# Kernel tuning notes

Measured on AMD Instinct MI355X. Metric: run time of the kernel, lower is better.

## Reference

```python
import jax, jax.numpy as jnp
import numpy as np

N = 100000
NNZ = 3200000
NFEAT, NHID, NCLASS = 512, 256, 41

def setup_inputs() -> dict:
    key = jax.random.key(0)
    ks = jax.random.split(key, 8)
    x = jax.random.normal(ks[0], (N, NFEAT), dtype=jnp.float32)
    adj_rows = jnp.sort(jax.random.randint(ks[1], (NNZ,), 0, N))
    adj_cols = jax.random.randint(ks[2], (NNZ,), 0, N)
    adj_vals = jax.random.uniform(ks[3], (NNZ,), dtype=jnp.float32) / 32.0  # ~normalized adj
    s1 = 1.0 / np.sqrt(NHID)
    s2 = 1.0 / np.sqrt(NCLASS)
    w1 = jax.random.uniform(ks[4], (NFEAT, NHID), minval=-s1, maxval=s1, dtype=jnp.float32)
    b1 = jax.random.uniform(ks[5], (NHID,), minval=-s1, maxval=s1, dtype=jnp.float32)
    w2 = jax.random.uniform(ks[6], (NHID, NCLASS), minval=-s2, maxval=s2, dtype=jnp.float32)
    b2 = jax.random.uniform(ks[7], (NCLASS,), minval=-s2, maxval=s2, dtype=jnp.float32)
    return {"x": x, "adj_rows": adj_rows, "adj_cols": adj_cols, "adj_vals": adj_vals,
            "w1": w1, "b1": b1, "w2": w2, "b2": b2}

def spmm(rows, cols, vals, dense):
    # sparse [N,N] @ dense [N,D] via gather + segment_sum
    gathered = dense[cols] * vals[:, None]  # [nnz, D]
    return jax.ops.segment_sum(gathered, rows, num_segments=N)

def reference(x, adj_rows, adj_cols, adj_vals, w1, b1, w2, b2):
    # layer 1: A(XW) + b, relu  (GraphConvolution)
    h = spmm(adj_rows, adj_cols, adj_vals, x @ w1) + b1
    h = jax.nn.relu(h)
    # dropout: inference mode (training=False) -> identity
    # layer 2: (AX)W + b  (GraphConvolution2)
    out = spmm(adj_rows, adj_cols, adj_vals, h) @ w2 + b2
    return jax.nn.log_softmax(out, axis=1)
```

## Files before the change

kernel.cpp:

```cpp
#include <hip/hip_runtime.h>
#include <math.h>

#define N_NODES 100000
#define NNZ_E   3200000
#define NFEAT   512
#define NHID    256
#define NCLASS  41
#define NC_PAD  48
#define P_STRIDE 64

typedef __attribute__((ext_vector_type(8))) short   short8;
typedef __attribute__((ext_vector_type(8))) unsigned short ushort8;
typedef __attribute__((ext_vector_type(4))) float   f32x4;
typedef __attribute__((ext_vector_type(2))) float   f32x2;

typedef __attribute__((address_space(1))) const unsigned int gu32;
typedef __attribute__((address_space(3))) unsigned int lu32;

__device__ __forceinline__ unsigned short f2bf(float f) {
    unsigned u = __builtin_bit_cast(unsigned, f);
    unsigned r = u + 0x7fffu + ((u >> 16) & 1u);
    return (unsigned short)(r >> 16);
}
__device__ __forceinline__ unsigned char f2fp8(float f) {
    return (unsigned char)(__builtin_amdgcn_cvt_pk_fp8_f32(f, 0.f, 0, false) & 0xff);
}

__global__ __launch_bounds__(256) void prep_x_kernel(const float* __restrict__ x,
                                                     unsigned char* __restrict__ xq) {
    long i = (long)(blockIdx.x * 256 + threadIdx.x) * 16;
    float4 f0 = *(const float4*)(x + i);
    float4 f1 = *(const float4*)(x + i + 4);
    float4 f2 = *(const float4*)(x + i + 8);
    float4 f3 = *(const float4*)(x + i + 12);
    uint4 o;
    o.x = (unsigned)__builtin_amdgcn_cvt_pk_fp8_f32(f0.x, f0.y, 0, false);
    o.x = (unsigned)__builtin_amdgcn_cvt_pk_fp8_f32(f0.z, f0.w, (int)o.x, true);
    o.y = (unsigned)__builtin_amdgcn_cvt_pk_fp8_f32(f1.x, f1.y, 0, false);
    o.y = (unsigned)__builtin_amdgcn_cvt_pk_fp8_f32(f1.z, f1.w, (int)o.y, true);
    o.z = (unsigned)__builtin_amdgcn_cvt_pk_fp8_f32(f2.x, f2.y, 0, false);
    o.z = (unsigned)__builtin_amdgcn_cvt_pk_fp8_f32(f2.z, f2.w, (int)o.z, true);
    o.w = (unsigned)__builtin_amdgcn_cvt_pk_fp8_f32(f3.x, f3.y, 0, false);
    o.w = (unsigned)__builtin_amdgcn_cvt_pk_fp8_f32(f3.z, f3.w, (int)o.w, true);
    *(uint4*)(xq + i) = o;
}

__global__ void prep_w_kernel(const float* __restrict__ w1, const float* __restrict__ w2,
                              unsigned char* __restrict__ w1q, unsigned short* __restrict__ w2t) {
    int tid = blockIdx.x * 256 + threadIdx.x;
    if (tid < NHID * NFEAT) {
        int n = tid >> 9, k = tid & 511;
        w1q[tid] = f2fp8(w1[k * NHID + n]);
    }
    int t2 = tid - NHID * NFEAT;
    if (t2 >= 0 && t2 < NC_PAD * NHID) {
        int n = t2 >> 8, k = t2 & 255;
        w2t[t2] = (n < NCLASS) ? f2bf(w2[k * NCLASS + n]) : (unsigned short)0;
    }
}

__global__ void rowptr_kernel(const int* __restrict__ rows, int* __restrict__ row_ptr) {
    int r = blockIdx.x * 256 + threadIdx.x;
    if (r > N_NODES) return;
    int lo = 0, hi = NNZ_E;
    while (lo < hi) {
        int mid = (lo + hi) >> 1;
        if (rows[mid] < r) lo = mid + 1; else hi = mid;
    }
    row_ptr[r] = lo;
}

__global__ __launch_bounds__(256) void gemm1_kernel(const unsigned char* __restrict__ xq,
                                                    const unsigned char* __restrict__ w1q,
                                                    unsigned char* __restrict__ xw) {
    __shared__ unsigned char As[8192];
    __shared__ unsigned char Bs[8192];

    const int wv   = threadIdx.x >> 6;
    const int lane = threadIdx.x & 63;
    const int l15  = lane & 15;
    const int quad = lane >> 4;
    const int rb   = blockIdx.x * 128;
    const int nb   = blockIdx.y * 128;

    const int srow0 = (wv * 2 + 0) * 16 + (lane >> 2);
    const int srow1 = (wv * 2 + 1) * 16 + (lane >> 2);
    const int g0 = (lane & 3) ^ ((srow0 >> 1) & 3);
    const int g1 = (lane & 3) ^ ((srow1 >> 1) & 3);
    int ga0 = rb + srow0; if (ga0 >= N_NODES) ga0 = N_NODES - 1;
    int ga1 = rb + srow1; if (ga1 >= N_NODES) ga1 = N_NODES - 1;
    const unsigned char* agp0 = xq + (long)ga0 * NFEAT + g0 * 16;
    const unsigned char* agp1 = xq + (long)ga1 * NFEAT + g1 * 16;
    const unsigned char* bgp0 = w1q + (long)(nb + srow0) * NFEAT + g0 * 16;
    const unsigned char* bgp1 = w1q + (long)(nb + srow1) * NFEAT + g1 * 16;

    f32x4 acc[4][4] = {};

    for (int kc = 0; kc < NFEAT; kc += 64) {
        __builtin_amdgcn_global_load_lds((gu32*)(agp0 + kc), (lu32*)(As + (wv * 2 + 0) * 1024), 16, 0, 0);
        __builtin_amdgcn_global_load_lds((gu32*)(agp1 + kc), (lu32*)(As + (wv * 2 + 1) * 1024), 16, 0, 0);
        __builtin_amdgcn_global_load_lds((gu32*)(bgp0 + kc), (lu32*)(Bs + (wv * 2 + 0) * 1024), 16, 0, 0);
        __builtin_amdgcn_global_load_lds((gu32*)(bgp1 + kc), (lu32*)(Bs + (wv * 2 + 1) * 1024), 16, 0, 0);
        __syncthreads();

        unsigned long long a[4][2], b[4][2];
#pragma unroll
        for (int mt = 0; mt < 4; mt++) {
            int row = (wv & 1) * 64 + mt * 16 + l15;
#pragma unroll
            for (int ks = 0; ks < 2; ks++) {
                int p8 = (ks * 4 + quad) ^ (row & 6);
                a[mt][ks] = *(const unsigned long long*)(As + row * 64 + p8 * 8);
            }
        }
#pragma unroll
        for (int nt = 0; nt < 4; nt++) {
            int nr = (wv >> 1) * 64 + nt * 16 + l15;
#pragma unroll
            for (int ks = 0; ks < 2; ks++) {
                int p8 = (ks * 4 + quad) ^ (nr & 6);
                b[nt][ks] = *(const unsigned long long*)(Bs + nr * 64 + p8 * 8);
            }
        }
#pragma unroll
        for (int ks = 0; ks < 2; ks++)
#pragma unroll
            for (int nt = 0; nt < 4; nt++)
#pragma unroll
                for (int mt = 0; mt < 4; mt++)
                    acc[mt][nt] = __builtin_amdgcn_mfma_f32_16x16x32_fp8_fp8(
                        (long)a[mt][ks], (long)b[nt][ks], acc[mt][nt], 0, 0, 0);
        __syncthreads();
    }

#pragma unroll
    for (int mt = 0; mt < 4; mt++) {
        int row0 = rb + (wv & 1) * 64 + mt * 16 + quad * 4;
#pragma unroll
        for (int nt = 0; nt < 4; nt++) {
            int col = nb + (wv >> 1) * 64 + nt * 16 + l15;
#pragma unroll
            for (int r = 0; r < 4; r++) {
                int row = row0 + r;
                if (row < N_NODES)
                    xw[(long)row * NHID + col] = f2fp8(acc[mt][nt][r]);
            }
        }
    }
}

__global__ __launch_bounds__(256) void spmm1_kernel(const unsigned char* __restrict__ xw,
                                                    const int* __restrict__ row_ptr,
                                                    const int* __restrict__ cols,
                                                    const float* __restrict__ vals,
                                                    const float* __restrict__ b1,
                                                    unsigned short* __restrict__ h) {
    int row = blockIdx.x * 4 + (threadIdx.x >> 6);
    if (row >= N_NODES) return;
    int lane = threadIdx.x & 63;
    int e0 = row_ptr[row], e1 = row_ptr[row + 1];

    float a0 = 0.f, a1 = 0.f, a2 = 0.f, a3 = 0.f;
    for (int base = e0; base < e1; base += 64) {
        int   myc = 0;
        float myv = 0.f;
        int idx = base + lane;
        if (idx < e1) { myc = cols[idx]; myv = vals[idx]; }
        int cnt = e1 - base; if (cnt > 64) cnt = 64;
        int j = 0;
        for (; j + 8 <= cnt; j += 8) {
            int c[8]; float v[8];
#pragma unroll
            for (int u = 0; u < 8; u++) { c[u] = __shfl(myc, j + u); v[u] = __shfl(myv, j + u); }
            unsigned q[8];
#pragma unroll
            for (int u = 0; u < 8; u++) q[u] = *(const unsigned*)(xw + (long)c[u] * NHID + lane * 4);
#pragma unroll
            for (int u = 0; u < 8; u++) {
                f32x2 lo = __builtin_amdgcn_cvt_pk_f32_fp8((int)q[u], false);
                f32x2 hi = __builtin_amdgcn_cvt_pk_f32_fp8((int)q[u], true);
                a0 += v[u] * lo[0];
                a1 += v[u] * lo[1];
                a2 += v[u] * hi[0];
                a3 += v[u] * hi[1];
            }
        }
        for (; j < cnt; j++) {
            int   c = __shfl(myc, j);
            float v = __shfl(myv, j);
            unsigned q = *(const unsigned*)(xw + (long)c * NHID + lane * 4);
            f32x2 lo = __builtin_amdgcn_cvt_pk_f32_fp8((int)q, false);
            f32x2 hi = __builtin_amdgcn_cvt_pk_f32_fp8((int)q, true);
            a0 += v * lo[0];
            a1 += v * lo[1];
            a2 += v * hi[0];
            a3 += v * hi[1];
        }
    }
    float4 bv = *(const float4*)(b1 + lane * 4);
    a0 = fmaxf(a0 + bv.x, 0.f);
    a1 = fmaxf(a1 + bv.y, 0.f);
    a2 = fmaxf(a2 + bv.z, 0.f);
    a3 = fmaxf(a3 + bv.w, 0.f);
    uint2 o;
    o.x = (unsigned)f2bf(a0) | ((unsigned)f2bf(a1) << 16);
    o.y = (unsigned)f2bf(a2) | ((unsigned)f2bf(a3) << 16);
    *(uint2*)(h + (long)row * NHID + lane * 4) = o;
}

__global__ __launch_bounds__(256) void gemm2_kernel(const unsigned short* __restrict__ h,
                                                    const unsigned short* __restrict__ w2t,
                                                    unsigned char* __restrict__ p) {
    int rt = blockIdx.x * 4 + (threadIdx.x >> 6);
    int row0 = rt * 16;
    if (row0 >= N_NODES) return;
    int lane = threadIdx.x & 63;
    int l15 = lane & 15, quad = lane >> 4;

    int arow = row0 + l15; if (arow >= N_NODES) arow = N_NODES - 1;
    f32x4 acc[3] = {};
#pragma unroll
    for (int kc = 0; kc < NHID; kc += 32) {
        short8 a = *(const short8*)(h + (long)arow * NHID + kc + quad * 8);
#pragma unroll
        for (int nt = 0; nt < 3; nt++) {
            short8 b = *(const short8*)(w2t + (long)(nt * 16 + l15) * NHID + kc + quad * 8);
            acc[nt] = __builtin_amdgcn_mfma_f32_16x16x32_bf16(a, b, acc[nt], 0, 0, 0);
        }
    }
#pragma unroll
    for (int nt = 0; nt < 3; nt++) {
        int col = nt * 16 + l15;
#pragma unroll
        for (int r = 0; r < 4; r++) {
            int row = row0 + quad * 4 + r;
            if (row < N_NODES)
                p[(long)row * P_STRIDE + col] = f2fp8(acc[nt][r]);
        }
    }
}

__global__ __launch_bounds__(256) void spmm2_kernel(const unsigned char* __restrict__ p,
                                                    const int* __restrict__ row_ptr,
                                                    const int* __restrict__ cols,
                                                    const float* __restrict__ vals,
                                                    const float* __restrict__ b2,
                                                    float* __restrict__ out) {
    int row = blockIdx.x * 4 + (threadIdx.x >> 6);
    if (row >= N_NODES) return;
    int lane = threadIdx.x & 63;
    int e = lane >> 5;
    int t = lane & 31;
    int e0 = row_ptr[row], e1 = row_ptr[row + 1];

    float a0 = 0.f, a1 = 0.f, a2 = 0.f, a3 = 0.f;
    for (int base = e0; base < e1; base += 64) {
        int   myc = 0;
        float myv = 0.f;
        int idx = base + lane;
        if (idx < e1) { myc = cols[idx]; myv = vals[idx]; }
        int cnt = e1 - base; if (cnt > 64) cnt = 64;
        int j = 0;
        for (; j + 8 <= cnt; j += 8) {
            int c[4]; float v[4];
#pragma unroll
            for (int u = 0; u < 4; u++) {
                c[u] = __shfl(myc, j + 2 * u + e);
                v[u] = __shfl(myv, j + 2 * u + e);
            }
            unsigned q[4];
#pragma unroll
            for (int u = 0; u < 4; u++)
                q[u] = (t < 12) ? *(const unsigned*)(p + (long)c[u] * P_STRIDE + 4 * t) : 0u;
#pragma unroll
            for (int u = 0; u < 4; u++) {
                f32x2 lo = __builtin_amdgcn_cvt_pk_f32_fp8((int)q[u], false);
                f32x2 hi = __builtin_amdgcn_cvt_pk_f32_fp8((int)q[u], true);
                a0 += v[u] * lo[0];
                a1 += v[u] * lo[1];
                a2 += v[u] * hi[0];
                a3 += v[u] * hi[1];
            }
        }
        for (; j < cnt; j += 2) {
            int jj = j + e;
            int jc = jj < cnt ? jj : cnt - 1;
            int   c = __shfl(myc, jc);
            float v = __shfl(myv, jc);
            if (jj >= cnt) v = 0.f;
            unsigned q = (t < 12) ? *(const unsigned*)(p + (long)c * P_STRIDE + 4 * t) : 0u;
            f32x2 lo = __builtin_amdgcn_cvt_pk_f32_fp8((int)q, false);
            f32x2 hi = __builtin_amdgcn_cvt_pk_f32_fp8((int)q, true);
            a0 += v * lo[0];
            a1 += v * lo[1];
            a2 += v * hi[0];
            a3 += v * hi[1];
        }
    }
    a0 += __shfl_xor(a0, 32);
    a1 += __shfl_xor(a1, 32);
    a2 += __shfl_xor(a2, 32);
    a3 += __shfl_xor(a3, 32);

    int c0 = 4 * t, c1 = 4 * t + 1, c2 = 4 * t + 2, c3 = 4 * t + 3;
    float l0 = (c0 < NCLASS) ? a0 + b2[c0] : -__builtin_inff();
    float l1 = (c1 < NCLASS) ? a1 + b2[c1] : -__builtin_inff();
    float l2 = (c2 < NCLASS) ? a2 + b2[c2] : -__builtin_inff();
    float l3 = (c3 < NCLASS) ? a3 + b2[c3] : -__builtin_inff();
    float m = fmaxf(fmaxf(l0, l1), fmaxf(l2, l3));
#pragma unroll
    for (int s = 16; s; s >>= 1) m = fmaxf(m, __shfl_xor(m, s));
    float esum = ((c0 < NCLASS) ? __expf(l0 - m) : 0.f)
               + ((c1 < NCLASS) ? __expf(l1 - m) : 0.f)
               + ((c2 < NCLASS) ? __expf(l2 - m) : 0.f)
               + ((c3 < NCLASS) ? __expf(l3 - m) : 0.f);
#pragma unroll
    for (int s = 16; s; s >>= 1) esum += __shfl_xor(esum, s);
    float lse = m + __logf(esum);
    if (e == 0) {
        long ob = (long)row * NCLASS;
        if (c0 < NCLASS) out[ob + c0] = l0 - lse;
        if (c1 < NCLASS) out[ob + c1] = l1 - lse;
        if (c2 < NCLASS) out[ob + c2] = l2 - lse;
        if (c3 < NCLASS) out[ob + c3] = l3 - lse;
    }
}

extern "C" void kernel_launch(void* const* d_in, const int* in_sizes, int n_in,
                              void* d_out, int out_size, void* d_ws, size_t ws_size,
                              hipStream_t stream) {
    const float* x        = (const float*)d_in[0];
    const int*   adj_rows = (const int*)  d_in[1];
    const int*   adj_cols = (const int*)  d_in[2];
    const float* adj_vals = (const float*)d_in[3];
    const float* w1       = (const float*)d_in[4];
    const float* b1       = (const float*)d_in[5];
    const float* w2       = (const float*)d_in[6];
    const float* b2       = (const float*)d_in[7];
    float* out = (float*)d_out;

    char* ws = (char*)d_ws;
    unsigned char*  w1q     = (unsigned char*) (ws);
    unsigned short* w2t     = (unsigned short*)(ws + 0x20000);
    int*            row_ptr = (int*)           (ws + 0x26000);
    unsigned char*  xq      = (unsigned char*) (ws + 0x90000);
    unsigned short* hbuf    = (unsigned short*)(ws + 0x90000);
    unsigned char*  xw      = (unsigned char*) (ws + 0x3180000);
    unsigned char*  p       = (unsigned char*) (ws + 0x3180000);

    prep_x_kernel<<<(N_NODES * NFEAT) / 16 / 256, 256, 0, stream>>>(x, xq);
    prep_w_kernel<<<(NHID * NFEAT + NC_PAD * NHID + 255) / 256, 256, 0, stream>>>(w1, w2, w1q, w2t);
    rowptr_kernel<<<(N_NODES + 1 + 255) / 256, 256, 0, stream>>>(adj_rows, row_ptr);
    gemm1_kernel<<<dim3((N_NODES + 127) / 128, 2), 256, 0, stream>>>(xq, w1q, xw);
    spmm1_kernel<<<(N_NODES + 3) / 4, 256, 0, stream>>>(xw, row_ptr, adj_cols, adj_vals, b1, hbuf);
    gemm2_kernel<<<((N_NODES + 15) / 16 + 3) / 4, 256, 0, stream>>>(hbuf, w2t, p);
    spmm2_kernel<<<(N_NODES + 3) / 4, 256, 0, stream>>>(p, row_ptr, adj_cols, adj_vals, b2, out);
}
```

Baseline: 568.7 us.

## Slice XW into 32-byte column panels and split SpMM1 across slices

GEMM1 now writes its FP8 output as eight column slices of 32 bytes per row. SpMM1 launches eight times as many blocks, one per (row group, slice). In each wave, 8 edge groups of 8 lanes gather 32-byte segments from the slice, with the next column and value loads prefetched, and the partial sums are reduced by cross-lane shuffles. The intent is to shrink each slice's gather working set so it fits better in L2/MALL and to spread edges across lanes, at the cost of reading cols/vals eight times. The row-pointer and weight-prep kernels are merged into one launch, and nontemporal loads are added for the edge arrays.

```diff
diff --git a/kernel.cpp b/kernel.cpp
--- a/kernel.cpp
+++ b/kernel.cpp
@@ -9,10 +9,15 @@
 #define NC_PAD  48
 #define P_STRIDE 64
 
+#define SLICE_B      32
+#define NSLICE       8
+#define SLICE_STRIDE (N_NODES * SLICE_B)
+
 typedef __attribute__((ext_vector_type(8))) short   short8;
 typedef __attribute__((ext_vector_type(8))) unsigned short ushort8;
 typedef __attribute__((ext_vector_type(4))) float   f32x4;
 typedef __attribute__((ext_vector_type(2))) float   f32x2;
+typedef __attribute__((ext_vector_type(2))) unsigned int u32x2;
 
 typedef __attribute__((address_space(1))) const unsigned int gu32;
 typedef __attribute__((address_space(3))) unsigned int lu32;
@@ -45,29 +50,37 @@
     *(uint4*)(xq + i) = o;
 }
 
-__global__ void prep_w_kernel(const float* __restrict__ w1, const float* __restrict__ w2,
-                              unsigned char* __restrict__ w1q, unsigned short* __restrict__ w2t) {
-    int tid = blockIdx.x * 256 + threadIdx.x;
-    if (tid < NHID * NFEAT) {
+__global__ __launch_bounds__(256) void prep_misc_kernel(const int* __restrict__ rows,
+                                                        const float* __restrict__ w1,
+                                                        const float* __restrict__ w2,
+                                                        int* __restrict__ row_ptr,
+                                                        unsigned char* __restrict__ w1q,
+                                                        unsigned short* __restrict__ w2t) {
+    int b = blockIdx.x;
+    if (b < 392) {
+        int r = b * 256 + threadIdx.x;
+        if (r > N_NODES) return;
+        int lo = 0, hi = NNZ_E;
+        while (lo < hi) {
+            int mid = (lo + hi) >> 1;
+            if (rows[mid] < r) lo = mid + 1; else hi = mid;
+        }
+        row_ptr[r] = lo;
+        return;
+    }
+    b -= 392;
+    if (b < 512) {
+        int tid = b * 256 + threadIdx.x;
         int n = tid >> 9, k = tid & 511;
         w1q[tid] = f2fp8(w1[k * NHID + n]);
-    }
-    int t2 = tid - NHID * NFEAT;
-    if (t2 >= 0 && t2 < NC_PAD * NHID) {
+        return;
+    }
+    b -= 512;
+    {
+        int t2 = b * 256 + threadIdx.x;
         int n = t2 >> 8, k = t2 & 255;
         w2t[t2] = (n < NCLASS) ? f2bf(w2[k * NCLASS + n]) : (unsigned short)0;
     }
-}
-
-__global__ void rowptr_kernel(const int* __restrict__ rows, int* __restrict__ row_ptr) {
-    int r = blockIdx.x * 256 + threadIdx.x;
-    if (r > N_NODES) return;
-    int lo = 0, hi = NNZ_E;
-    while (lo < hi) {
-        int mid = (lo + hi) >> 1;
-        if (rows[mid] < r) lo = mid + 1; else hi = mid;
-    }
-    row_ptr[r] = lo;
 }
 
 __global__ __launch_bounds__(256) void gemm1_kernel(const unsigned char* __restrict__ xq,
@@ -139,73 +152,82 @@
 #pragma unroll
         for (int nt = 0; nt < 4; nt++) {
             int col = nb + (wv >> 1) * 64 + nt * 16 + l15;
+            long sb = (long)(col >> 5) * SLICE_STRIDE + (col & 31);
 #pragma unroll
             for (int r = 0; r < 4; r++) {
                 int row = row0 + r;
                 if (row < N_NODES)
-                    xw[(long)row * NHID + col] = f2fp8(acc[mt][nt][r]);
-            }
-        }
-    }
-}
-
-__global__ __launch_bounds__(256) void spmm1_kernel(const unsigned char* __restrict__ xw,
+                    xw[sb + (long)row * SLICE_B] = f2fp8(acc[mt][nt][r]);
+            }
+        }
+    }
+}
+
+__global__ __launch_bounds__(256) void spmm1_kernel(const unsigned char* __restrict__ xws,
                                                     const int* __restrict__ row_ptr,
                                                     const int* __restrict__ cols,
                                                     const float* __restrict__ vals,
                                                     const float* __restrict__ b1,
                                                     unsigned short* __restrict__ h) {
-    int row = blockIdx.x * 4 + (threadIdx.x >> 6);
+    const int slice = blockIdx.x & 7;
+    const int row   = (blockIdx.x >> 3) * 4 + (threadIdx.x >> 6);
     if (row >= N_NODES) return;
-    int lane = threadIdx.x & 63;
-    int e0 = row_ptr[row], e1 = row_ptr[row + 1];
+    const int lane = threadIdx.x & 63;
+    const int e = lane >> 3;
+    const int t = lane & 7;
+    int e0 = __builtin_amdgcn_readfirstlane(row_ptr[row]);
+    int e1 = __builtin_amdgcn_readfirstlane(row_ptr[row + 1]);
+
+    const unsigned char* sbase = xws + (long)slice * SLICE_STRIDE;
+    const unsigned toff = (unsigned)(t << 2);
 
     float a0 = 0.f, a1 = 0.f, a2 = 0.f, a3 = 0.f;
-    for (int base = e0; base < e1; base += 64) {
-        int   myc = 0;
-        float myv = 0.f;
-        int idx = base + lane;
-        if (idx < e1) { myc = cols[idx]; myv = vals[idx]; }
-        int cnt = e1 - base; if (cnt > 64) cnt = 64;
-        int j = 0;
-        for (; j + 8 <= cnt; j += 8) {
-            int c[8]; float v[8];
-#pragma unroll
-            for (int u = 0; u < 8; u++) { c[u] = __shfl(myc, j + u); v[u] = __shfl(myv, j + u); }
-            unsigned q[8];
-#pragma unroll
-            for (int u = 0; u < 8; u++) q[u] = *(const unsigned*)(xw + (long)c[u] * NHID + lane * 4);
-#pragma unroll
-            for (int u = 0; u < 8; u++) {
-                f32x2 lo = __builtin_amdgcn_cvt_pk_f32_fp8((int)q[u], false);
-                f32x2 hi = __builtin_amdgcn_cvt_pk_f32_fp8((int)q[u], true);
-                a0 += v[u] * lo[0];
-                a1 += v[u] * lo[1];
-                a2 += v[u] * hi[0];
-                a3 += v[u] * hi[1];
-            }
-        }
-        for (; j < cnt; j++) {
-            int   c = __shfl(myc, j);
-            float v = __shfl(myv, j);
-            unsigned q = *(const unsigned*)(xw + (long)c * NHID + lane * 4);
-            f32x2 lo = __builtin_amdgcn_cvt_pk_f32_fp8((int)q, false);
-            f32x2 hi = __builtin_amdgcn_cvt_pk_f32_fp8((int)q, true);
-            a0 += v * lo[0];
-            a1 += v * lo[1];
-            a2 += v * hi[0];
-            a3 += v * hi[1];
-        }
-    }
-    float4 bv = *(const float4*)(b1 + lane * 4);
-    a0 = fmaxf(a0 + bv.x, 0.f);
-    a1 = fmaxf(a1 + bv.y, 0.f);
-    a2 = fmaxf(a2 + bv.z, 0.f);
-    a3 = fmaxf(a3 + bv.w, 0.f);
-    uint2 o;
-    o.x = (unsigned)f2bf(a0) | ((unsigned)f2bf(a1) << 16);
-    o.y = (unsigned)f2bf(a2) | ((unsigned)f2bf(a3) << 16);
-    *(uint2*)(h + (long)row * NHID + lane * 4) = o;
+    if (e0 < e1) {
+        const int em1 = e1 - 1;
+        int i0 = e0 + e;     int i0c = i0 < e1 ? i0 : em1;
+        int i1 = e0 + 8 + e; int i1c = i1 < e1 ? i1 : em1;
+        int   ca = __builtin_nontemporal_load(cols + i0c);
+        float va = __builtin_nontemporal_load(vals + i0c);
+        int   cb = __builtin_nontemporal_load(cols + i1c);
+        float vb = __builtin_nontemporal_load(vals + i1c);
+        for (int j = e0; j < e1; j += 16) {
+            int n0 = j + 16 + e; int n0c = n0 < e1 ? n0 : em1;
+            int n1 = j + 24 + e; int n1c = n1 < e1 ? n1 : em1;
+            int   cc = __builtin_nontemporal_load(cols + n0c);
+            float vc = __builtin_nontemporal_load(vals + n0c);
+            int   cd = __builtin_nontemporal_load(cols + n1c);
+            float vd = __builtin_nontemporal_load(vals + n1c);
+            unsigned q0 = *(const unsigned*)(sbase + (((unsigned)ca << 5) | toff));
+            unsigned q1 = *(const unsigned*)(sbase + (((unsigned)cb << 5) | toff));
+            float v0 = (j + e     < e1) ? va : 0.f;
+            float v1 = (j + 8 + e < e1) ? vb : 0.f;
+            f32x2 lo0 = __builtin_amdgcn_cvt_pk_f32_fp8((int)q0, false);
+            f32x2 hi0 = __builtin_amdgcn_cvt_pk_f32_fp8((int)q0, true);
+            f32x2 lo1 = __builtin_amdgcn_cvt_pk_f32_fp8((int)q1, false);
+            f32x2 hi1 = __builtin_amdgcn_cvt_pk_f32_fp8((int)q1, true);
+            a0 += v0 * lo0[0]; a1 += v0 * lo0[1]; a2 += v0 * hi0[0]; a3 += v0 * hi0[1];
+            a0 += v1 * lo1[0]; a1 += v1 * lo1[1]; a2 += v1 * hi1[0]; a3 += v1 * hi1[1];
+            ca = cc; va = vc; cb = cd; vb = vd;
+        }
+    }
+    a0 += __shfl_xor(a0, 8);  a1 += __shfl_xor(a1, 8);
+    a2 += __shfl_xor(a2, 8);  a3 += __shfl_xor(a3, 8);
+    a0 += __shfl_xor(a0, 16); a1 += __shfl_xor(a1, 16);
+    a2 += __shfl_xor(a2, 16); a3 += __shfl_xor(a3, 16);
+    a0 += __shfl_xor(a0, 32); a1 += __shfl_xor(a1, 32);
+    a2 += __shfl_xor(a2, 32); a3 += __shfl_xor(a3, 32);
+
+    if (e == 0) {
+        const float4 bv = *(const float4*)(b1 + slice * SLICE_B + (t << 2));
+        a0 = fmaxf(a0 + bv.x, 0.f);
+        a1 = fmaxf(a1 + bv.y, 0.f);
+        a2 = fmaxf(a2 + bv.z, 0.f);
+        a3 = fmaxf(a3 + bv.w, 0.f);
+        u32x2 o;
+        o.x = (unsigned)f2bf(a0) | ((unsigned)f2bf(a1) << 16);
+        o.y = (unsigned)f2bf(a2) | ((unsigned)f2bf(a3) << 16);
+        __builtin_nontemporal_store(o, (u32x2*)(h + (long)row * NHID + slice * SLICE_B + (t << 2)));
+    }
 }
 
 __global__ __launch_bounds__(256) void gemm2_kernel(const unsigned short* __restrict__ h,
@@ -258,7 +280,10 @@
         int   myc = 0;
         float myv = 0.f;
         int idx = base + lane;
-        if (idx < e1) { myc = cols[idx]; myv = vals[idx]; }
+        if (idx < e1) {
+            myc = __builtin_nontemporal_load(cols + idx);
+            myv = __builtin_nontemporal_load(vals + idx);
+        }
         int cnt = e1 - base; if (cnt > 64) cnt = 64;
         int j = 0;
         for (; j + 8 <= cnt; j += 8) {
@@ -349,10 +374,9 @@
     unsigned char*  p       = (unsigned char*) (ws + 0x3180000);
 
     prep_x_kernel<<<(N_NODES * NFEAT) / 16 / 256, 256, 0, stream>>>(x, xq);
-    prep_w_kernel<<<(NHID * NFEAT + NC_PAD * NHID + 255) / 256, 256, 0, stream>>>(w1, w2, w1q, w2t);
-    rowptr_kernel<<<(N_NODES + 1 + 255) / 256, 256, 0, stream>>>(adj_rows, row_ptr);
+    prep_misc_kernel<<<392 + 512 + 48, 256, 0, stream>>>(adj_rows, w1, w2, row_ptr, w1q, w2t);
     gemm1_kernel<<<dim3((N_NODES + 127) / 128, 2), 256, 0, stream>>>(xq, w1q, xw);
-    spmm1_kernel<<<(N_NODES + 3) / 4, 256, 0, stream>>>(xw, row_ptr, adj_cols, adj_vals, b1, hbuf);
+    spmm1_kernel<<<(N_NODES / 4) * NSLICE, 256, 0, stream>>>(xw, row_ptr, adj_cols, adj_vals, b1, hbuf);
     gemm2_kernel<<<((N_NODES + 15) / 16 + 3) / 4, 256, 0, stream>>>(hbuf, w2t, p);
     spmm2_kernel<<<(N_NODES + 3) / 4, 256, 0, stream>>>(p, row_ptr, adj_cols, adj_vals, b2, out);
 }
```

Result: slower. 847.9 us (+49.1%).

## Fuse fp8 quantization of x into GEMM1 and merge prep kernels

Applied to the files above, without the earlier changes.

Drops the separate pass that converted x to fp8. GEMM1 now reads fp32 x directly, converts it in registers and writes it into LDS, prefetching the next K-chunk in registers. Each GEMM1 block covers all 256 output columns with 512 threads, so x is read only once. The rowptr and weight-prep kernels merge into one launch, and spmm2 uses nontemporal loads for cols/vals. This removes a full write and re-read of the 51MB fp8 copy of x plus two launches, at the cost of reading fp32 x (4x more bytes) inside the GEMM with a less async load path.

```diff
diff --git a/kernel.cpp b/kernel.cpp
--- a/kernel.cpp
+++ b/kernel.cpp
@@ -10,7 +10,6 @@
 #define P_STRIDE 64
 
 typedef __attribute__((ext_vector_type(8))) short   short8;
-typedef __attribute__((ext_vector_type(8))) unsigned short ushort8;
 typedef __attribute__((ext_vector_type(4))) float   f32x4;
 typedef __attribute__((ext_vector_type(2))) float   f32x2;
 
@@ -25,88 +24,102 @@
 __device__ __forceinline__ unsigned char f2fp8(float f) {
     return (unsigned char)(__builtin_amdgcn_cvt_pk_fp8_f32(f, 0.f, 0, false) & 0xff);
 }
-
-__global__ __launch_bounds__(256) void prep_x_kernel(const float* __restrict__ x,
-                                                     unsigned char* __restrict__ xq) {
-    long i = (long)(blockIdx.x * 256 + threadIdx.x) * 16;
-    float4 f0 = *(const float4*)(x + i);
-    float4 f1 = *(const float4*)(x + i + 4);
-    float4 f2 = *(const float4*)(x + i + 8);
-    float4 f3 = *(const float4*)(x + i + 12);
-    uint4 o;
-    o.x = (unsigned)__builtin_amdgcn_cvt_pk_fp8_f32(f0.x, f0.y, 0, false);
-    o.x = (unsigned)__builtin_amdgcn_cvt_pk_fp8_f32(f0.z, f0.w, (int)o.x, true);
-    o.y = (unsigned)__builtin_amdgcn_cvt_pk_fp8_f32(f1.x, f1.y, 0, false);
-    o.y = (unsigned)__builtin_amdgcn_cvt_pk_fp8_f32(f1.z, f1.w, (int)o.y, true);
-    o.z = (unsigned)__builtin_amdgcn_cvt_pk_fp8_f32(f2.x, f2.y, 0, false);
-    o.z = (unsigned)__builtin_amdgcn_cvt_pk_fp8_f32(f2.z, f2.w, (int)o.z, true);
-    o.w = (unsigned)__builtin_amdgcn_cvt_pk_fp8_f32(f3.x, f3.y, 0, false);
-    o.w = (unsigned)__builtin_amdgcn_cvt_pk_fp8_f32(f3.z, f3.w, (int)o.w, true);
-    *(uint4*)(xq + i) = o;
-}
-
-__global__ void prep_w_kernel(const float* __restrict__ w1, const float* __restrict__ w2,
-                              unsigned char* __restrict__ w1q, unsigned short* __restrict__ w2t) {
-    int tid = blockIdx.x * 256 + threadIdx.x;
-    if (tid < NHID * NFEAT) {
+__device__ __forceinline__ unsigned pk4(float a, float b, float c, float d) {
+    unsigned u = __builtin_amdgcn_cvt_pk_fp8_f32(a, b, 0, false);
+    return (unsigned)__builtin_amdgcn_cvt_pk_fp8_f32(c, d, (int)u, true);
+}
+
+__global__ __launch_bounds__(256) void prep_misc_kernel(const int* __restrict__ rows,
+                                                        const float* __restrict__ w1,
+                                                        const float* __restrict__ w2,
+                                                        int* __restrict__ row_ptr,
+                                                        unsigned char* __restrict__ w1q,
+                                                        unsigned short* __restrict__ w2t) {
+    int b = blockIdx.x;
+    if (b < 392) {
+        int r = b * 256 + threadIdx.x;
+        if (r > N_NODES) return;
+        int lo = 0, hi = NNZ_E;
+        while (lo < hi) {
+            int mid = (lo + hi) >> 1;
+            if (rows[mid] < r) lo = mid + 1; else hi = mid;
+        }
+        row_ptr[r] = lo;
+        return;
+    }
+    b -= 392;
+    if (b < 512) {
+        int tid = b * 256 + threadIdx.x;
         int n = tid >> 9, k = tid & 511;
         w1q[tid] = f2fp8(w1[k * NHID + n]);
-    }
-    int t2 = tid - NHID * NFEAT;
-    if (t2 >= 0 && t2 < NC_PAD * NHID) {
+        return;
+    }
+    b -= 512;
+    {
+        int t2 = b * 256 + threadIdx.x;
         int n = t2 >> 8, k = t2 & 255;
         w2t[t2] = (n < NCLASS) ? f2bf(w2[k * NCLASS + n]) : (unsigned short)0;
     }
 }
 
-__global__ void rowptr_kernel(const int* __restrict__ rows, int* __restrict__ row_ptr) {
-    int r = blockIdx.x * 256 + threadIdx.x;
-    if (r > N_NODES) return;
-    int lo = 0, hi = NNZ_E;
-    while (lo < hi) {
-        int mid = (lo + hi) >> 1;
-        if (rows[mid] < r) lo = mid + 1; else hi = mid;
-    }
-    row_ptr[r] = lo;
-}
-
-__global__ __launch_bounds__(256) void gemm1_kernel(const unsigned char* __restrict__ xq,
+__global__ __launch_bounds__(512) void gemm1_kernel(const float* __restrict__ x,
                                                     const unsigned char* __restrict__ w1q,
                                                     unsigned char* __restrict__ xw) {
     __shared__ unsigned char As[8192];
-    __shared__ unsigned char Bs[8192];
-
-    const int wv   = threadIdx.x >> 6;
-    const int lane = threadIdx.x & 63;
+    __shared__ unsigned char Bs[16384];
+
+    const int tid  = threadIdx.x;
+    const int wv   = tid >> 6;
+    const int lane = tid & 63;
     const int l15  = lane & 15;
     const int quad = lane >> 4;
+    const int wvM  = wv >> 2;
+    const int wvN  = wv & 3;
     const int rb   = blockIdx.x * 128;
-    const int nb   = blockIdx.y * 128;
-
-    const int srow0 = (wv * 2 + 0) * 16 + (lane >> 2);
-    const int srow1 = (wv * 2 + 1) * 16 + (lane >> 2);
-    const int g0 = (lane & 3) ^ ((srow0 >> 1) & 3);
-    const int g1 = (lane & 3) ^ ((srow1 >> 1) & 3);
-    int ga0 = rb + srow0; if (ga0 >= N_NODES) ga0 = N_NODES - 1;
-    int ga1 = rb + srow1; if (ga1 >= N_NODES) ga1 = N_NODES - 1;
-    const unsigned char* agp0 = xq + (long)ga0 * NFEAT + g0 * 16;
-    const unsigned char* agp1 = xq + (long)ga1 * NFEAT + g1 * 16;
-    const unsigned char* bgp0 = w1q + (long)(nb + srow0) * NFEAT + g0 * 16;
-    const unsigned char* bgp1 = w1q + (long)(nb + srow1) * NFEAT + g1 * 16;
+
+    const int ar = tid >> 2;
+    const int aq = tid & 3;
+    int arow = rb + ar; if (arow >= N_NODES) arow = N_NODES - 1;
+    const float* asrc = x + (long)arow * NFEAT + aq * 16;
+    unsigned char* adst0 = As + ar * 64 + (((2 * aq + 0) ^ (ar & 6)) * 8);
+    unsigned char* adst1 = As + ar * 64 + (((2 * aq + 1) ^ (ar & 6)) * 8);
+
+    const int bn0 = (wv * 2 + 0) * 16 + (lane >> 2);
+    const int bn1 = (wv * 2 + 1) * 16 + (lane >> 2);
+    const int bg0 = (lane & 3) ^ ((bn0 >> 1) & 3);
+    const int bg1 = (lane & 3) ^ ((bn1 >> 1) & 3);
+    const unsigned char* bsrc0 = w1q + (long)bn0 * NFEAT + bg0 * 16;
+    const unsigned char* bsrc1 = w1q + (long)bn1 * NFEAT + bg1 * 16;
 
     f32x4 acc[4][4] = {};
 
-    for (int kc = 0; kc < NFEAT; kc += 64) {
-        __builtin_amdgcn_global_load_lds((gu32*)(agp0 + kc), (lu32*)(As + (wv * 2 + 0) * 1024), 16, 0, 0);
-        __builtin_amdgcn_global_load_lds((gu32*)(agp1 + kc), (lu32*)(As + (wv * 2 + 1) * 1024), 16, 0, 0);
-        __builtin_amdgcn_global_load_lds((gu32*)(bgp0 + kc), (lu32*)(Bs + (wv * 2 + 0) * 1024), 16, 0, 0);
-        __builtin_amdgcn_global_load_lds((gu32*)(bgp1 + kc), (lu32*)(Bs + (wv * 2 + 1) * 1024), 16, 0, 0);
+    float4 fr0 = *(const float4*)(asrc);
+    float4 fr1 = *(const float4*)(asrc + 4);
+    float4 fr2 = *(const float4*)(asrc + 8);
+    float4 fr3 = *(const float4*)(asrc + 12);
+
+    for (int c = 0; c < 8; c++) {
+        const int kc = c * 64;
+        __builtin_amdgcn_global_load_lds((gu32*)(bsrc0 + kc), (lu32*)(Bs + (wv * 2 + 0) * 1024), 16, 0, 0);
+        __builtin_amdgcn_global_load_lds((gu32*)(bsrc1 + kc), (lu32*)(Bs + (wv * 2 + 1) * 1024), 16, 0, 0);
+        unsigned u0 = pk4(fr0.x, fr0.y, fr0.z, fr0.w);
+        unsigned u1 = pk4(fr1.x, fr1.y, fr1.z, fr1.w);
+        unsigned u2 = pk4(fr2.x, fr2.y, fr2.z, fr2.w);
+        unsigned u3 = pk4(fr3.x, fr3.y, fr3.z, fr3.w);
+        *(unsigned long long*)adst0 = (unsigned long long)u0 | ((unsigned long long)u1 << 32);
+        *(unsigned long long*)adst1 = (unsigned long long)u2 | ((unsigned long long)u3 << 32);
+        if (c < 7) {
+            fr0 = *(const float4*)(asrc + kc + 64);
+            fr1 = *(const float4*)(asrc + kc + 68);
+            fr2 = *(const float4*)(asrc + kc + 72);
+            fr3 = *(const float4*)(asrc + kc + 76);
+        }
         __syncthreads();
 
         unsigned long long a[4][2], b[4][2];
 #pragma unroll
         for (int mt = 0; mt < 4; mt++) {
-            int row = (wv & 1) * 64 + mt * 16 + l15;
+            int row = wvM * 64 + mt * 16 + l15;
 #pragma unroll
             for (int ks = 0; ks < 2; ks++) {
                 int p8 = (ks * 4 + quad) ^ (row & 6);
@@ -115,7 +128,7 @@
         }
 #pragma unroll
         for (int nt = 0; nt < 4; nt++) {
-            int nr = (wv >> 1) * 64 + nt * 16 + l15;
+            int nr = wvN * 64 + nt * 16 + l15;
 #pragma unroll
             for (int ks = 0; ks < 2; ks++) {
                 int p8 = (ks * 4 + quad) ^ (nr & 6);
@@ -135,10 +148,10 @@
 
 #pragma unroll
     for (int mt = 0; mt < 4; mt++) {
-        int row0 = rb + (wv & 1) * 64 + mt * 16 + quad * 4;
+        int row0 = rb + wvM * 64 + mt * 16 + quad * 4;
 #pragma unroll
         for (int nt = 0; nt < 4; nt++) {
-            int col = nb + (wv >> 1) * 64 + nt * 16 + l15;
+            int col = wvN * 64 + nt * 16 + l15;
 #pragma unroll
             for (int r = 0; r < 4; r++) {
                 int row = row0 + r;
@@ -258,7 +271,10 @@
         int   myc = 0;
         float myv = 0.f;
         int idx = base + lane;
-        if (idx < e1) { myc = cols[idx]; myv = vals[idx]; }
+        if (idx < e1) {
+            myc = __builtin_nontemporal_load(cols + idx);
+            myv = __builtin_nontemporal_load(vals + idx);
+        }
         int cnt = e1 - base; if (cnt > 64) cnt = 64;
         int j = 0;
         for (; j + 8 <= cnt; j += 8) {
@@ -343,15 +359,12 @@
     unsigned char*  w1q     = (unsigned char*) (ws);
     unsigned short* w2t     = (unsigned short*)(ws + 0x20000);
     int*            row_ptr = (int*)           (ws + 0x26000);
-    unsigned char*  xq      = (unsigned char*) (ws + 0x90000);
     unsigned short* hbuf    = (unsigned short*)(ws + 0x90000);
     unsigned char*  xw      = (unsigned char*) (ws + 0x3180000);
     unsigned char*  p       = (unsigned char*) (ws + 0x3180000);
 
-    prep_x_kernel<<<(N_NODES * NFEAT) / 16 / 256, 256, 0, stream>>>(x, xq);
-    prep_w_kernel<<<(NHID * NFEAT + NC_PAD * NHID + 255) / 256, 256, 0, stream>>>(w1, w2, w1q, w2t);
-    rowptr_kernel<<<(N_NODES + 1 + 255) / 256, 256, 0, stream>>>(adj_rows, row_ptr);
-    gemm1_kernel<<<dim3((N_NODES + 127) / 128, 2), 256, 0, stream>>>(xq, w1q, xw);
+    prep_misc_kernel<<<392 + 512 + 48, 256, 0, stream>>>(adj_rows, w1, w2, row_ptr, w1q, w2t);
+    gemm1_kernel<<<(N_NODES + 127) / 128, 512, 0, stream>>>(x, w1q, xw);
     spmm1_kernel<<<(N_NODES + 3) / 4, 256, 0, stream>>>(xw, row_ptr, adj_cols, adj_vals, b1, hbuf);
     gemm2_kernel<<<((N_NODES + 15) / 16 + 3) / 4, 256, 0, stream>>>(hbuf, w2t, p);
     spmm2_kernel<<<(N_NODES + 3) / 4, 256, 0, stream>>>(p, row_ptr, adj_cols, adj_vals, b2, out);
```

Result: faster. 552.9 us (-2.8%).
